# Kernel tuning notes

Measured on AMD Instinct MI355X. Metric: run time of the kernel, lower is better.

## Reference

```python
import jax, jax.numpy as jnp
import numpy as np

T_SCALES = [0.0, 0.25, 0.5, 0.75, 1.0]  # ODEblock time_scales; Euler step per consecutive pair
NUM_ZEROS = 10
BETA = 0.6  # defined in ODEFunc but unused in its forward


def _odefunc(x, x0, adj, alpha, w, d, w2, d2):
    # x: [B, N, T, Fa]; adj: [N, N]; alpha: [N]; w: [Fa, Fa]; d: [Fa]; w2: [T, T]; d2: [T]
    a = jax.nn.sigmoid(alpha)[None, :, None, None]              # [1, N, 1, 1]
    xa = jnp.einsum('ij,kjln->kiln', adj, x)                    # adjacency propagation over nodes
    dc = jnp.clip(d, 0.0, 1.0)
    W = (w * dc) @ w.T                                          # [Fa, Fa]
    # NOTE: faithful to torch source: 'ijkl,mn->ijkm' has NO shared contraction
    # index => xw = (sum_l x) outer (sum_n W) — reproduced exactly.
    xw = jnp.einsum('ijkl,mn->ijkm', x, W)
    d2c = jnp.clip(d2, 0.0, 1.0)
    W2 = (w2 * d2c) @ w2.T                                      # [T, T]
    xw2 = jnp.einsum('ijkl,kn->ijnl', x, W2)                    # temporal mixing
    # f = alpha/2*xa - x + xw - x + xw2 - x + x0
    return a * 0.5 * xa - 3.0 * x + xw + xw2 + x0


def setup_inputs() -> dict:
    key = jax.random.key(0)
    k1, k2 = jax.random.split(key)
    B, N, T, F = 32, 512, 24, 64
    Fa = F + NUM_ZEROS
    x = jax.random.normal(k1, (B, N, T, F), dtype=jnp.float32)
    adj = jax.random.uniform(k2, (N, N), dtype=jnp.float32) / N  # normalized dense adjacency
    alpha = 0.8 * jnp.ones((N,), jnp.float32)                    # nn.Parameter init 0.8*ones
    w = jnp.eye(Fa, dtype=jnp.float32)                           # nn.Parameter init eye
    d = jnp.ones((Fa,), jnp.float32)                             # nn.Parameter init ones
    w2 = jnp.eye(T, dtype=jnp.float32)
    d2 = jnp.ones((T,), jnp.float32)
    return {"x": x, "adj": adj, "alpha": alpha, "w": w, "d": d, "w2": w2, "d2": d2}


def reference(x, adj, alpha, w, d, w2, d2):
    B, N, T, F = x.shape
    if F == 64:
        x_aug = jnp.concatenate(
            [x, jnp.zeros((B, N, T, NUM_ZEROS), dtype=x.dtype)], axis=3)
    else:
        x_aug = x
    x0 = jax.lax.stop_gradient(x_aug)  # set_x0 uses clone().detach()
    # Euler odeint with two time points does one step: z = x + dt * f(x).
    # Original loop restarts from x_aug each iteration, so f is constant.
    f = _odefunc(x_aug, x0, adj, alpha, w, d, w2, d2)
    z = x_aug
    for i in range(len(T_SCALES) - 1):
        dt = T_SCALES[i + 1] - T_SCALES[i]
        z = x_aug + dt * f  # overwrites z each iteration, as in the torch code
    return jax.nn.relu(z)
```

## Files before the change

kernel.cpp:

```cpp
#include <hip/hip_runtime.h>
#include <hip/hip_fp16.h>
#include <cstdint>
#include <cstddef>

#define B_  32
#define N_  512
#define T_  24
#define F_  64
#define FA_ 74
#define NC  1536

typedef __attribute__((ext_vector_type(8))) _Float16 half8;
typedef __attribute__((ext_vector_type(8))) unsigned short ushort8;
typedef __attribute__((ext_vector_type(4))) float floatx4;

#define WS_ADJ 1536
#define WS_XT  132608

#define AS1(p) ((const __attribute__((address_space(1))) void*)(p))
#define AS3(p) ((__attribute__((address_space(3))) void*)(p))

union h2u { _Float16 h; unsigned short u; };

__global__ __launch_bounds__(256) void prep_kernel(
    const float* __restrict__ x, const float* __restrict__ adj,
    const float* __restrict__ alpha, const float* __restrict__ w,
    const float* __restrict__ d, const float* __restrict__ w2,
    const float* __restrict__ d2, float* __restrict__ ws) {
  __shared__ float tile[64 * 65];
  __shared__ float cs[FA_];
  int bid = blockIdx.x;
  int tid = threadIdx.x;
  if (bid < 6144) {
    _Float16* xT = (_Float16*)(ws + WS_XT);
    int ct = bid % 24;
    int kt = (bid / 24) % 8;
    int b = bid / 192;
    int c0 = ct * 64;
    int k0 = kt * 64;
#pragma unroll
    for (int it = 0; it < 4; ++it) {
      int g = it * 256 + tid;
      int k = g >> 4, c4 = g & 15;
      float4 v = *(const float4*)&x[((size_t)(b * N_ + k0 + k)) * NC + c0 + c4 * 4];
      tile[k * 65 + c4 * 4 + 0] = v.x;
      tile[k * 65 + c4 * 4 + 1] = v.y;
      tile[k * 65 + c4 * 4 + 2] = v.z;
      tile[k * 65 + c4 * 4 + 3] = v.w;
    }
    __syncthreads();
#pragma unroll
    for (int it = 0; it < 4; ++it) {
      int hh = it * 256 + tid;
      int c = hh >> 4, k4 = hh & 15;
      ushort4 u4; h2u cv;
      cv.h = (_Float16)tile[(k4 * 4 + 0) * 65 + c]; u4.x = cv.u;
      cv.h = (_Float16)tile[(k4 * 4 + 1) * 65 + c]; u4.y = cv.u;
      cv.h = (_Float16)tile[(k4 * 4 + 2) * 65 + c]; u4.z = cv.u;
      cv.h = (_Float16)tile[(k4 * 4 + 3) * 65 + c]; u4.w = cv.u;
      *(ushort4*)&xT[((size_t)b * NC + c0 + c) * 512 + k0 + k4 * 4] = u4;
    }
  } else if (bid < 6400) {
    _Float16* adjH = (_Float16*)(ws + WS_ADJ);
    int g = ((bid - 6144) * 256 + tid) * 4;
    int row = g >> 9;
    float sc = 0.125f / (1.f + __expf(-alpha[row]));
    float4 v = *(const float4*)&adj[g];
    ushort4 u4; h2u cv;
    cv.h = (_Float16)(sc * v.x); u4.x = cv.u;
    cv.h = (_Float16)(sc * v.y); u4.y = cv.u;
    cv.h = (_Float16)(sc * v.z); u4.z = cv.u;
    cv.h = (_Float16)(sc * v.w); u4.w = cv.u;
    *(ushort4*)&adjH[g] = u4;
  } else {
    if (tid < FA_) {
      float s = 0.f;
      for (int n = 0; n < FA_; ++n) s += w[n * FA_ + tid];
      cs[tid] = s;
    }
    __syncthreads();
    if (tid < FA_) {
      float s = 0.f;
      for (int p = 0; p < FA_; ++p) {
        float dc = fminf(fmaxf(d[p], 0.f), 1.f);
        s += w[tid * FA_ + p] * dc * cs[p];
      }
      ws[tid] = s;
    }
    for (int e = tid; e < T_ * T_; e += 256) {
      int a = e / T_, b = e % T_;
      float s = 0.f;
      for (int p = 0; p < T_; ++p) {
        float dc = fminf(fmaxf(d2[p], 0.f), 1.f);
        s += w2[a * T_ + p] * dc * w2[b * T_ + p];
      }
      ws[128 + e] = s;
    }
  }
}

__global__ __launch_bounds__(256) void gemm_kernel(
    const float* __restrict__ ws, const float* __restrict__ x,
    float* __restrict__ out) {
  const _Float16* adjH = (const _Float16*)(ws + WS_ADJ);
  const _Float16* xT   = (const _Float16*)(ws + WS_XT);

  __shared__ __align__(16) char smem[33792];
  _Float16* As = (_Float16*)smem;
  _Float16* Bs = (_Float16*)(smem + 16384);
  float* accS = (float*)smem;
  __shared__ float coefs[48];

  int raw = blockIdx.x;
  int nid = (raw & 7) * 192 + (raw >> 3);
  int iq = nid & 3;
  int rest = nid >> 2;
  int cb = rest % 12;
  int b = rest / 12;
  int i0 = iq * 128;
  int c0 = cb * 128;
  int t0 = cb * 2;

  int tid = threadIdx.x;
  int wave = tid >> 6, lane = tid & 63;
  int mw = (wave & 1) * 64, nw = (wave >> 1) * 64;
  int l15 = lane & 15, l4 = lane >> 4;

  if (tid < 48) {
    int tl = tid / 24, tp = tid - (tid / 24) * 24;
    float cf = 0.25f * ws[128 + (t0 + tl) * 24 + tp];
    if (tp == t0 + tl) cf += 0.5f;
    coefs[tid] = cf;
  }

  floatx4 acc[4][4];
#pragma unroll
  for (int mt = 0; mt < 4; ++mt)
#pragma unroll
    for (int nt = 0; nt < 4; ++nt) acc[mt][nt] = (floatx4){0.f, 0.f, 0.f, 0.f};

  const size_t bC = (size_t)b * NC;
  for (int k0 = 0; k0 < 512; k0 += 64) {
#pragma unroll
    for (int rep = 0; rep < 4; ++rep) {
      int chunk = rep * 256 + tid;
      int r = chunk >> 3;
      int s = chunk & 7;
      int ss = (s ^ (r & 7)) * 8;
      __builtin_amdgcn_global_load_lds(AS1(adjH + (size_t)(i0 + r) * 512 + k0 + ss),
                                       AS3(&As[chunk * 8]), 16, 0, 0);
      __builtin_amdgcn_global_load_lds(AS1(xT + (bC + c0 + r) * 512 + k0 + ss),
                                       AS3(&Bs[chunk * 8]), 16, 0, 0);
    }
    __syncthreads();
#pragma unroll
    for (int ks = 0; ks < 2; ++ks) {
      half8 af[4], bfv[4];
#pragma unroll
      for (int mt = 0; mt < 4; ++mt) {
        int row = mw + mt * 16 + l15;
        int slot = (ks * 4 + l4) ^ (row & 7);
        af[mt] = *(const half8*)&As[row * 64 + slot * 8];
      }
#pragma unroll
      for (int nt = 0; nt < 4; ++nt) {
        int row = nw + nt * 16 + l15;
        int slot = (ks * 4 + l4) ^ (row & 7);
        bfv[nt] = *(const half8*)&Bs[row * 64 + slot * 8];
      }
#pragma unroll
      for (int mt = 0; mt < 4; ++mt)
#pragma unroll
        for (int nt = 0; nt < 4; ++nt)
          acc[mt][nt] = __builtin_amdgcn_mfma_f32_16x16x32_f16(af[mt], bfv[nt], acc[mt][nt], 0, 0, 0);
    }
    __syncthreads();
  }

  const size_t bN = (size_t)b * N_;
  int f = tid & 63;
  int rj = tid >> 6;
  float rsWf = ws[f];
  float rsWa = (f < 10) ? ws[64 + f] : 0.f;
  for (int h = 0; h < 2; ++h) {
    if ((wave & 1) == h) {
#pragma unroll
      for (int mt = 0; mt < 4; ++mt)
#pragma unroll
        for (int nt = 0; nt < 4; ++nt)
#pragma unroll
          for (int r = 0; r < 4; ++r)
            accS[(mt * 16 + l4 * 4 + r) * 132 + nw + nt * 16 + l15] = acc[mt][nt][r];
    }
    __syncthreads();

#pragma unroll 2
    for (int jj = 0; jj < 16; ++jj) {
      int row = rj + 4 * jj;
      int grow = i0 + h * 64 + row;
      const float* xr = x + (bN + grow) * NC;
      float xv[24];
#pragma unroll
      for (int tp = 0; tp < 24; ++tp) xv[tp] = xr[tp * 64 + f];
      float s0 = xv[t0], s1 = xv[t0 + 1];
#pragma unroll
      for (int off = 32; off >= 1; off >>= 1) {
        s0 += __shfl_xor(s0, off, 64);
        s1 += __shfl_xor(s1, off, 64);
      }
      float tm0 = 0.f, tm1 = 0.f;
#pragma unroll
      for (int tp = 0; tp < 24; ++tp) {
        tm0 += coefs[tp] * xv[tp];
        tm1 += coefs[24 + tp] * xv[tp];
      }
      float v0 = accS[row * 132 + f]      + tm0 + 0.25f * s0 * rsWf;
      float v1 = accS[row * 132 + 64 + f] + tm1 + 0.25f * s1 * rsWf;
      size_t o = ((bN + grow) * T_ + t0) * FA_ + f;
      out[o] = fmaxf(v0, 0.f);
      out[o + FA_] = fmaxf(v1, 0.f);
      if (f < 10) {
        out[o + 64] = fmaxf(0.25f * s0 * rsWa, 0.f);
        out[o + FA_ + 64] = fmaxf(0.25f * s1 * rsWa, 0.f);
      }
    }
    __syncthreads();
  }
}

extern "C" void kernel_launch(void* const* d_in, const int* in_sizes, int n_in,
                              void* d_out, int out_size, void* d_ws, size_t ws_size,
                              hipStream_t stream) {
  const float* x     = (const float*)d_in[0];
  const float* adj   = (const float*)d_in[1];
  const float* alpha = (const float*)d_in[2];
  const float* w     = (const float*)d_in[3];
  const float* d     = (const float*)d_in[4];
  const float* w2    = (const float*)d_in[5];
  const float* d2    = (const float*)d_in[6];
  float* out = (float*)d_out;
  float* ws  = (float*)d_ws;

  hipLaunchKernelGGL(prep_kernel, dim3(6401), dim3(256), 0, stream,
                     x, adj, alpha, w, d, w2, d2, ws);
  hipLaunchKernelGGL(gemm_kernel, dim3(1536), dim3(256), 0, stream, ws, x, out);
}
```

Before: 318.1 us.

## Precompute per-row feature sums in prep and vectorize GEMM epilogue

The prep kernel now computes per-(batch, time, node) sums over the 64 features while the x tile is already in shared memory, and stores them in workspace. The GEMM epilogue reads those sums instead of doing a 64-lane shuffle reduction, and processes rows with float4 loads and stores over 16 feature groups. It also spills the whole accumulator tile to shared memory in one pass instead of two halves. This doubles shared memory per block, which may lower occupancy, and adds a small workspace write in prep.

```diff
diff --git a/kernel.cpp b/kernel.cpp
--- a/kernel.cpp
+++ b/kernel.cpp
@@ -13,9 +13,11 @@
 typedef __attribute__((ext_vector_type(8))) _Float16 half8;
 typedef __attribute__((ext_vector_type(8))) unsigned short ushort8;
 typedef __attribute__((ext_vector_type(4))) float floatx4;
+typedef __attribute__((ext_vector_type(2))) float floatx2;
 
 #define WS_ADJ 1536
 #define WS_XT  132608
+#define WS_S   12715520
 
 #define AS1(p) ((const __attribute__((address_space(1))) void*)(p))
 #define AS3(p) ((__attribute__((address_space(3))) void*)(p))
@@ -33,6 +35,7 @@
   int tid = threadIdx.x;
   if (bid < 6144) {
     _Float16* xT = (_Float16*)(ws + WS_XT);
+    float* Sp = ws + WS_S;
     int ct = bid % 24;
     int kt = (bid / 24) % 8;
     int b = bid / 192;
@@ -49,6 +52,15 @@
       tile[k * 65 + c4 * 4 + 3] = v.w;
     }
     __syncthreads();
+    {
+      int k = tid >> 2, q = tid & 3;
+      float s = 0.f;
+#pragma unroll
+      for (int j = 0; j < 16; ++j) s += tile[k * 65 + q * 16 + j];
+      s += __shfl_xor(s, 1, 64);
+      s += __shfl_xor(s, 2, 64);
+      if (q == 0) Sp[((size_t)b * T_ + ct) * N_ + k0 + k] = s;
+    }
 #pragma unroll
     for (int it = 0; it < 4; ++it) {
       int hh = it * 256 + tid;
@@ -104,8 +116,9 @@
     float* __restrict__ out) {
   const _Float16* adjH = (const _Float16*)(ws + WS_ADJ);
   const _Float16* xT   = (const _Float16*)(ws + WS_XT);
-
-  __shared__ __align__(16) char smem[33792];
+  const float* Sp      = ws + WS_S;
+
+  __shared__ __align__(16) char smem[67584];
   _Float16* As = (_Float16*)smem;
   _Float16* Bs = (_Float16*)(smem + 16384);
   float* accS = (float*)smem;
@@ -177,54 +190,56 @@
     __syncthreads();
   }
 
+#pragma unroll
+  for (int mt = 0; mt < 4; ++mt)
+#pragma unroll
+    for (int nt = 0; nt < 4; ++nt)
+#pragma unroll
+      for (int r = 0; r < 4; ++r)
+        accS[(mw + mt * 16 + l4 * 4 + r) * 132 + nw + nt * 16 + l15] = acc[mt][nt][r];
+  __syncthreads();
+
   const size_t bN = (size_t)b * N_;
-  int f = tid & 63;
-  int rj = tid >> 6;
-  float rsWf = ws[f];
-  float rsWa = (f < 10) ? ws[64 + f] : 0.f;
-  for (int h = 0; h < 2; ++h) {
-    if ((wave & 1) == h) {
-#pragma unroll
-      for (int mt = 0; mt < 4; ++mt)
-#pragma unroll
-        for (int nt = 0; nt < 4; ++nt)
-#pragma unroll
-          for (int r = 0; r < 4; ++r)
-            accS[(mt * 16 + l4 * 4 + r) * 132 + nw + nt * 16 + l15] = acc[mt][nt][r];
-    }
-    __syncthreads();
+  int fq = tid & 15;
+  int rslot = tid >> 4;
+  floatx4 rsW4 = *(const floatx4*)&ws[fq * 4];
+  float rsWa = (fq < 10) ? ws[64 + fq] : 0.f;
+  const float* SpT = Sp + ((size_t)b * T_ + t0) * N_;
 
 #pragma unroll 2
-    for (int jj = 0; jj < 16; ++jj) {
-      int row = rj + 4 * jj;
-      int grow = i0 + h * 64 + row;
-      const float* xr = x + (bN + grow) * NC;
-      float xv[24];
-#pragma unroll
-      for (int tp = 0; tp < 24; ++tp) xv[tp] = xr[tp * 64 + f];
-      float s0 = xv[t0], s1 = xv[t0 + 1];
-#pragma unroll
-      for (int off = 32; off >= 1; off >>= 1) {
-        s0 += __shfl_xor(s0, off, 64);
-        s1 += __shfl_xor(s1, off, 64);
-      }
-      float tm0 = 0.f, tm1 = 0.f;
-#pragma unroll
-      for (int tp = 0; tp < 24; ++tp) {
-        tm0 += coefs[tp] * xv[tp];
-        tm1 += coefs[24 + tp] * xv[tp];
-      }
-      float v0 = accS[row * 132 + f]      + tm0 + 0.25f * s0 * rsWf;
-      float v1 = accS[row * 132 + 64 + f] + tm1 + 0.25f * s1 * rsWf;
-      size_t o = ((bN + grow) * T_ + t0) * FA_ + f;
-      out[o] = fmaxf(v0, 0.f);
-      out[o + FA_] = fmaxf(v1, 0.f);
-      if (f < 10) {
-        out[o + 64] = fmaxf(0.25f * s0 * rsWa, 0.f);
-        out[o + FA_ + 64] = fmaxf(0.25f * s1 * rsWa, 0.f);
-      }
-    }
-    __syncthreads();
+  for (int ii = 0; ii < 8; ++ii) {
+    int row = ii * 16 + rslot;
+    int grow = i0 + row;
+    const float* xr = x + (bN + grow) * NC + fq * 4;
+    floatx4 xv[24];
+#pragma unroll
+    for (int tp = 0; tp < 24; ++tp) xv[tp] = *(const floatx4*)&xr[tp * 64];
+    float s0 = SpT[grow];
+    float s1 = SpT[N_ + grow];
+    floatx4 tm0 = (floatx4){0.f, 0.f, 0.f, 0.f};
+    floatx4 tm1 = (floatx4){0.f, 0.f, 0.f, 0.f};
+#pragma unroll
+    for (int tp = 0; tp < 24; ++tp) {
+      tm0 += coefs[tp] * xv[tp];
+      tm1 += coefs[24 + tp] * xv[tp];
+    }
+    floatx4 a0 = *(const floatx4*)&accS[row * 132 + fq * 4];
+    floatx4 a1 = *(const floatx4*)&accS[row * 132 + 64 + fq * 4];
+    floatx4 v0 = a0 + tm0 + (0.25f * s0) * rsW4;
+    floatx4 v1 = a1 + tm1 + (0.25f * s1) * rsW4;
+#pragma unroll
+    for (int j = 0; j < 4; ++j) {
+      v0[j] = fmaxf(v0[j], 0.f);
+      v1[j] = fmaxf(v1[j], 0.f);
+    }
+    size_t ob = ((bN + grow) * T_ + t0) * FA_;
+    *(floatx4*)&out[ob + fq * 4] = v0;
+    *(floatx2*)&out[ob + FA_ + fq * 4]     = (floatx2){v1[0], v1[1]};
+    *(floatx2*)&out[ob + FA_ + fq * 4 + 2] = (floatx2){v1[2], v1[3]};
+    if (fq < 10) {
+      out[ob + 64 + fq]       = fmaxf(0.25f * s0 * rsWa, 0.f);
+      out[ob + FA_ + 64 + fq] = fmaxf(0.25f * s1 * rsWa, 0.f);
+    }
   }
 }
 
```

After: 491.0 us. +54.4%, slower.
